# Optimization experiments

Measured on AMD Instinct MI355X. Metric: run time of the kernel, lower is better.

Reference implementation:

```python
import jax, jax.numpy as jnp
import numpy as np

N = 262144        # tokens routed
D = 1024          # input_dim
E = 64            # num_experts
TOP_K = 2
NOISE_EPS = 1e-05
ALPHA = 10.0


def setup_inputs() -> dict:
    key = jax.random.key(0)
    k1, k2, k3, k4, k5 = jax.random.split(key, 5)
    x = jax.random.normal(k1, (N, D), dtype=jnp.float32)
    # nn.Linear init scale ~ 1/sqrt(fan_in); keep logits at sane magnitude
    gate_w = jax.random.normal(k2, (E, D), dtype=jnp.float32) * (1.0 / np.sqrt(D))
    gate_b = jax.random.normal(k3, (E,), dtype=jnp.float32) * 0.01
    # w_noise is initialized to zeros in the module; use small random values
    # so the noise path is exercised
    w_noise = jax.random.normal(k4, (E, E), dtype=jnp.float32) * 0.01
    noise = jax.random.normal(k5, (N, E), dtype=jnp.float32)  # torch.randn_like
    return {"x": x, "gate_w": gate_w, "gate_b": gate_b,
            "w_noise": w_noise, "noise": noise}


def reference(x, gate_w, gate_b, w_noise, noise):
    # gate linear: [N, D] @ [D, E] + [E]
    clean_logits = jnp.einsum('nd,ed->ne', x, gate_w) + gate_b
    # training-mode learnable noise injection
    raw_noise_stddev = clean_logits @ w_noise                 # [N, E]
    noise_stddev = jax.nn.softplus(raw_noise_stddev) + NOISE_EPS
    logits = clean_logits + noise * noise_stddev              # noisy_logits

    # decompostion_tp: k-th largest per row (kthvalue(n - k + 1) == k-th largest)
    kth_largest = jax.lax.top_k(logits, TOP_K)[0][:, -1]       # [N]
    mask = logits < kth_largest[:, None]                       # strictly below kth
    sm = jax.nn.softmax(logits, axis=1)
    out = jnp.where(mask,
                    ALPHA * jnp.log1p(sm),      # alpha * log(sm + 1)
                    ALPHA * jnp.expm1(sm))      # alpha * (exp(sm) - 1)

    gates = jax.nn.softmax(out, axis=1)
    return gates
```

## Files before the change

kernel.cpp:

```cpp
#include <hip/hip_runtime.h>

typedef _Float16 half8v __attribute__((ext_vector_type(8)));
typedef float f32x4 __attribute__((ext_vector_type(4)));

constexpr float INV4096 = 1.0f / 4096.0f;
constexpr float ALPHA = 10.0f;

__device__ __forceinline__ f32x4 mfma16(half8v a, half8v b, f32x4 c_) {
  return __builtin_amdgcn_mfma_f32_16x16x32_f16(a, b, c_, 0, 0, 0);
}
__device__ __forceinline__ void dma16(const void *g, void *l) {
  __builtin_amdgcn_global_load_lds(
      (const __attribute__((address_space(1))) void *)g,
      (__attribute__((address_space(3))) void *)l, 16, 0, 0);
}
template <int N> __device__ __forceinline__ void wait_vm() {
  asm volatile("s_waitcnt vmcnt(%0)" ::"n"(N) : "memory");
}
#define FENCE() asm volatile("" ::: "memory")
#define BAR()                            \
  do {                                   \
    __builtin_amdgcn_s_barrier();        \
    __builtin_amdgcn_sched_barrier(0);   \
  } while (0)

__global__ __launch_bounds__(256) void presplit(const float *__restrict__ GW,
                                                const float *__restrict__ WN,
                                                char *__restrict__ ws) {
  const int b = blockIdx.x;
  const int tid = threadIdx.x;
  if (b < 64) {
    int idx = b * 256 + tid;
    int e = idx >> 8;
    int c4 = idx & 255;
    f32x4 v = *reinterpret_cast<const f32x4 *>(GW + (size_t)idx * 4);
#pragma unroll
    for (int j = 0; j < 4; ++j) {
      int k = c4 * 4 + j;
      float vv = v[j];
      _Float16 hh = (_Float16)vv;
      _Float16 ll = (_Float16)((vv - (float)hh) * 4096.0f);
      int ck = k >> 6, kk = k & 63;
      int off = ck * 16384 + e * 128 + ((((kk >> 3) ^ (e & 7))) << 4) + ((kk & 7) << 1);
      *reinterpret_cast<_Float16 *>(ws + off) = hh;
      *reinterpret_cast<_Float16 *>(ws + off + 8192) = ll;
    }
  } else {
    int idx = (b - 64) * 256 + tid;
    int k = idx >> 4;
    int e0 = (idx & 15) << 2;
    f32x4 v = *reinterpret_cast<const f32x4 *>(WN + (size_t)k * 64 + e0);
#pragma unroll
    for (int j = 0; j < 4; ++j) {
      int e = e0 + j;
      float vv = v[j];
      _Float16 hh = (_Float16)vv;
      _Float16 ll = (_Float16)((vv - (float)hh) * 4096.0f);
      int off = 262144 + e * 128 + ((((k >> 3) ^ (e & 7))) << 4) + ((k & 7) << 1);
      *reinterpret_cast<_Float16 *>(ws + off) = hh;
      *reinterpret_cast<_Float16 *>(ws + off + 8192) = ll;
    }
  }
}

__global__ __launch_bounds__(512, 4) void topk_gating(
    const float *__restrict__ X, const char *__restrict__ WS,
    const float *__restrict__ GB, const float *__restrict__ NZ,
    float *__restrict__ OUT) {
  __shared__ __align__(16) char lds[49152];
  const int tid = threadIdx.x;
  const int lane = tid & 63;
  const int wv = tid >> 6;
  const int q = lane >> 4;
  const int c = lane & 15;
  const int waveRow = blockIdx.x * 128 + wv * 16;

  f32x4 accH[4] = {};
  f32x4 accX[4] = {};
  f32x4 a0[4], a1[4];

  const float *xBase = X + (size_t)(waveRow + c) * 1024 + q * 8;
  const char *wsL = WS + wv * 2048 + lane * 16;

#define LDA4(dst, p)                        \
  {                                         \
    dst[0] = *(const f32x4 *)((p) + 0);     \
    dst[1] = *(const f32x4 *)((p) + 4);     \
    dst[2] = *(const f32x4 *)((p) + 32);    \
    dst[3] = *(const f32x4 *)((p) + 36);    \
  }
#define BDMA(CK)                                                      \
  {                                                                   \
    char *bd_ = lds + ((CK) % 3) * 16384 + wv * 2048;                 \
    dma16(wsL + (CK) * 16384, bd_);                                   \
    dma16(wsL + (CK) * 16384 + 1024, bd_ + 1024);                     \
  }
#define CONV(A, ah, al)                                           \
  {                                                               \
    _Pragma("unroll") for (int ks_ = 0; ks_ < 2; ++ks_)           \
        _Pragma("unroll") for (int j_ = 0; j_ < 8; ++j_) {        \
      float xv_ = A[ks_ * 2 + (j_ >> 2)][j_ & 3];                 \
      _Float16 hh_ = (_Float16)xv_;                               \
      ah[ks_][j_] = hh_;                                          \
      al[ks_][j_] = (_Float16)((xv_ - (float)hh_) * 4096.0f);     \
    }                                                             \
  }
#define MFMAB(BUF, ah, al)                                                 \
  {                                                                        \
    _Pragma("unroll") for (int ks_ = 0; ks_ < 2; ++ks_)                    \
        _Pragma("unroll") for (int t_ = 0; t_ < 4; ++t_) {                 \
      int e_ = t_ * 16 + c;                                                \
      int off_ = (BUF) + e_ * 128 + ((((ks_ * 4 + q) ^ (e_ & 7))) << 4);   \
      half8v bh_ = *reinterpret_cast<half8v *>(lds + off_);                \
      half8v bl_ = *reinterpret_cast<half8v *>(lds + off_ + 8192);         \
      accH[t_] = mfma16(ah[ks_], bh_, accH[t_]);                           \
      accX[t_] = mfma16(ah[ks_], bl_, accX[t_]);                           \
      accX[t_] = mfma16(al[ks_], bh_, accX[t_]);                           \
    }                                                                      \
  }
#define STEP(N, AC, AN)                                          \
  {                                                              \
    half8v ah[2], al[2];                                         \
    if ((N) + 1 <= 15) LDA4(AN, xBase + ((N) + 1) * 64);         \
    FENCE();                                                     \
    if ((N) + 2 <= 15) BDMA((N) + 2);                            \
    FENCE();                                                     \
    CONV(AC, ah, al);                                            \
    MFMAB(((N) % 3) * 16384, ah, al);                            \
  }

  BDMA(0); FENCE();
  LDA4(a0, xBase); FENCE();
  BDMA(1); FENCE();
  wait_vm<6>(); BAR();

  STEP(0, a0, a1)  wait_vm<6>(); BAR();
  STEP(1, a1, a0)  wait_vm<6>(); BAR();
  STEP(2, a0, a1)  wait_vm<6>(); BAR();
  STEP(3, a1, a0)  wait_vm<6>(); BAR();
  STEP(4, a0, a1)  wait_vm<6>(); BAR();
  STEP(5, a1, a0)  wait_vm<6>(); BAR();
  STEP(6, a0, a1)  wait_vm<6>(); BAR();
  STEP(7, a1, a0)  wait_vm<6>(); BAR();
  STEP(8, a0, a1)  wait_vm<6>(); BAR();
  STEP(9, a1, a0)  wait_vm<6>(); BAR();
  STEP(10, a0, a1) wait_vm<6>(); BAR();
  STEP(11, a1, a0) wait_vm<6>(); BAR();
  STEP(12, a0, a1) wait_vm<6>(); BAR();
  STEP(13, a1, a0) wait_vm<6>(); BAR();
  STEP(14, a0, a1) wait_vm<4>(); BAR();
  STEP(15, a1, a0)
  BAR();

  float bs0 = GB[c], bs1 = GB[16 + c], bs2 = GB[32 + c], bs3 = GB[48 + c];
  dma16(wsL + 262144, lds + 32768 + wv * 2048);
  dma16(wsL + 262144 + 1024, lds + 32768 + wv * 2048 + 1024);
  FENCE();
  float nz[4][4];
#pragma unroll
  for (int t = 0; t < 4; ++t)
#pragma unroll
    for (int r = 0; r < 4; ++r)
      nz[t][r] = NZ[(size_t)(waveRow + 4 * q + r) * 64 + t * 16 + c];

  float cl[4][4];
  const float bsv[4] = {bs0, bs1, bs2, bs3};
#pragma unroll
  for (int t = 0; t < 4; ++t)
#pragma unroll
    for (int r = 0; r < 4; ++r)
      cl[t][r] = accH[t][r] + accX[t][r] * INV4096 + bsv[t];

  char *cb = lds + wv * 4096;
#pragma unroll
  for (int t = 0; t < 4; ++t)
#pragma unroll
    for (int r = 0; r < 4; ++r) {
      int row = 4 * q + r;
      int colf = t * 16 + c;
      int off = row * 256 + ((((colf >> 2) ^ row)) << 4) + ((colf & 3) << 2);
      *reinterpret_cast<float *>(cb + off) = cl[t][r];
    }
  wait_vm<16>();
  BAR();

  f32x4 rH[4] = {};
  f32x4 rX[4] = {};
#pragma unroll
  for (int ks = 0; ks < 2; ++ks) {
    int slot0 = ks * 8 + q * 2;
    f32x4 va = *reinterpret_cast<f32x4 *>(cb + c * 256 + (((slot0 ^ c)) << 4));
    f32x4 vb = *reinterpret_cast<f32x4 *>(cb + c * 256 + ((((slot0 + 1) ^ c)) << 4));
    half8v ah, al;
#pragma unroll
    for (int j = 0; j < 4; ++j) {
      float v = va[j];
      _Float16 hh = (_Float16)v;
      ah[j] = hh;
      al[j] = (_Float16)((v - (float)hh) * 4096.0f);
      float v2 = vb[j];
      _Float16 h2 = (_Float16)v2;
      ah[4 + j] = h2;
      al[4 + j] = (_Float16)((v2 - (float)h2) * 4096.0f);
    }
#pragma unroll
    for (int t = 0; t < 4; ++t) {
      int e = t * 16 + c;
      int off = 32768 + e * 128 + ((((ks * 4 + q) ^ (e & 7))) << 4);
      half8v bh = *reinterpret_cast<half8v *>(lds + off);
      half8v bl = *reinterpret_cast<half8v *>(lds + off + 8192);
      rH[t] = mfma16(ah, bh, rH[t]);
      rX[t] = mfma16(ah, bl, rX[t]);
      rX[t] = mfma16(al, bh, rX[t]);
    }
  }

  float lg[4][4];
#pragma unroll
  for (int t = 0; t < 4; ++t)
#pragma unroll
    for (int r = 0; r < 4; ++r) {
      float raw = rH[t][r] + rX[t][r] * INV4096;
      float sp = fmaxf(raw, 0.0f) + __logf(1.0f + __expf(-fabsf(raw)));
      lg[r][t] = cl[t][r] + nz[t][r] * (sp + 1e-5f);
    }

#pragma unroll
  for (int r = 0; r < 4; ++r) {
    float v0 = lg[r][0], v1 = lg[r][1], v2 = lg[r][2], v3 = lg[r][3];
    float a = fmaxf(v0, v1), b_ = fminf(v0, v1);
    float d1 = fmaxf(v2, v3), d2 = fminf(v2, v3);
    float m1 = fmaxf(a, d1);
    float m2 = fmaxf(fminf(a, d1), fmaxf(b_, d2));
#pragma unroll
    for (int s = 1; s <= 8; s <<= 1) {
      float om1 = __shfl_xor(m1, s, 64);
      float om2 = __shfl_xor(m2, s, 64);
      float hi = fmaxf(m1, om1);
      float lo = fminf(m1, om1);
      float sec = (m1 >= om1) ? m2 : om2;
      m2 = fmaxf(lo, sec);
      m1 = hi;
    }
    float se[4], ssum = 0.f;
#pragma unroll
    for (int t = 0; t < 4; ++t) {
      se[t] = __expf(lg[r][t] - m1);
      ssum += se[t];
    }
#pragma unroll
    for (int s = 1; s <= 8; s <<= 1) ssum += __shfl_xor(ssum, s, 64);
    float inv = 1.0f / ssum;
    float ov[4];
#pragma unroll
    for (int t = 0; t < 4; ++t) {
      float sm = se[t] * inv;
      float vlog = ALPHA * __logf(1.0f + sm);
      float vexp = ALPHA * (__expf(sm) - 1.0f);
      ov[t] = (lg[r][t] < m2) ? vlog : vexp;
    }
    float g = fmaxf(fmaxf(ov[0], ov[1]), fmaxf(ov[2], ov[3]));
#pragma unroll
    for (int s = 1; s <= 8; s <<= 1) g = fmaxf(g, __shfl_xor(g, s, 64));
    float gsum = 0.f;
#pragma unroll
    for (int t = 0; t < 4; ++t) {
      ov[t] = __expf(ov[t] - g);
      gsum += ov[t];
    }
#pragma unroll
    for (int s = 1; s <= 8; s <<= 1) gsum += __shfl_xor(gsum, s, 64);
    float ginv = 1.0f / gsum;
    size_t rowOff = (size_t)(waveRow + 4 * q + r) * 64;
#pragma unroll
    for (int t = 0; t < 4; ++t)
      OUT[rowOff + t * 16 + c] = ov[t] * ginv;
  }
}

extern "C" void kernel_launch(void *const *d_in, const int *in_sizes, int n_in,
                              void *d_out, int out_size, void *d_ws,
                              size_t ws_size, hipStream_t stream) {
  const float *x = (const float *)d_in[0];
  const float *gw = (const float *)d_in[1];
  const float *gb = (const float *)d_in[2];
  const float *wn = (const float *)d_in[3];
  const float *nz = (const float *)d_in[4];
  float *out = (float *)d_out;
  char *ws = (char *)d_ws;
  const int N = in_sizes[0] / 1024;

  hipLaunchKernelGGL(presplit, dim3(68), dim3(256), 0, stream, gw, wn, ws);
  hipLaunchKernelGGL(topk_gating, dim3(N / 128), dim3(512), 0, stream, x, ws,
                     gb, nz, out);
}
```

Measured before the change: 270.5 us.

## Double-buffer 128-wide K chunks with half as many barriers

The K-loop now processes 128-element chunks in 8 steps instead of 64-element chunks in 16 steps. The weight tile is double-buffered in a 64KB LDS area instead of triple-buffered in 48KB, and the X tile is prefetched one step ahead into two register banks. Each block copies its whole weight chunk with thread-linear DMA addressing. This halves the barrier and waitcnt points per tile, which should cut synchronisation stalls. In exchange it raises per-block LDS and register use, which can lower the number of resident blocks per CU, and it shortens the weight prefetch distance from two steps to one.

```diff
diff --git a/kernel.cpp b/kernel.cpp
--- a/kernel.cpp
+++ b/kernel.cpp
@@ -67,7 +67,7 @@
     const float *__restrict__ X, const char *__restrict__ WS,
     const float *__restrict__ GB, const float *__restrict__ NZ,
     float *__restrict__ OUT) {
-  __shared__ __align__(16) char lds[49152];
+  __shared__ __align__(16) char lds[65536];
   const int tid = threadIdx.x;
   const int lane = tid & 63;
   const int wv = tid >> 6;
@@ -77,10 +77,10 @@
 
   f32x4 accH[4] = {};
   f32x4 accX[4] = {};
-  f32x4 a0[4], a1[4];
+  f32x4 aA[2][4], aB[2][4];
 
   const float *xBase = X + (size_t)(waveRow + c) * 1024 + q * 8;
-  const char *wsL = WS + wv * 2048 + lane * 16;
+  const char *wsT = WS + tid * 16;
 
 #define LDA4(dst, p)                        \
   {                                         \
@@ -89,11 +89,18 @@
     dst[2] = *(const f32x4 *)((p) + 32);    \
     dst[3] = *(const f32x4 *)((p) + 36);    \
   }
-#define BDMA(CK)                                                      \
-  {                                                                   \
-    char *bd_ = lds + ((CK) % 3) * 16384 + wv * 2048;                 \
-    dma16(wsL + (CK) * 16384, bd_);                                   \
-    dma16(wsL + (CK) * 16384 + 1024, bd_ + 1024);                     \
+#define LDAP(BANK, N)                       \
+  {                                         \
+    const float *p_ = xBase + (N) * 128;    \
+    LDA4(BANK[0], p_);                      \
+    LDA4(BANK[1], p_ + 64);                 \
+  }
+#define BDMA(N)                                                         \
+  {                                                                     \
+    char *bd_ = lds + ((N) % 2) * 32768;                                \
+    _Pragma("unroll") for (int i_ = 0; i_ < 4; ++i_)                    \
+        dma16(wsT + (N) * 32768 + i_ * 8192, bd_ + i_ * 8192 + tid * 16 \
+              - lane * 16);                                             \
   }
 #define CONV(A, ah, al)                                           \
   {                                                               \
@@ -118,43 +125,42 @@
       accX[t_] = mfma16(al[ks_], bh_, accX[t_]);                           \
     }                                                                      \
   }
-#define STEP(N, AC, AN)                                          \
-  {                                                              \
-    half8v ah[2], al[2];                                         \
-    if ((N) + 1 <= 15) LDA4(AN, xBase + ((N) + 1) * 64);         \
-    FENCE();                                                     \
-    if ((N) + 2 <= 15) BDMA((N) + 2);                            \
-    FENCE();                                                     \
-    CONV(AC, ah, al);                                            \
-    MFMAB(((N) % 3) * 16384, ah, al);                            \
+#define STEPC2(N, BANK)                                   \
+  {                                                       \
+    half8v ah[2], al[2];                                  \
+    CONV(BANK[0], ah, al);                                \
+    MFMAB(((N) % 2) * 32768, ah, al);                     \
+    CONV(BANK[1], ah, al);                                \
+    MFMAB(((N) % 2) * 32768 + 16384, ah, al);             \
+  }
+#define STEP(N, CUR, NXT)                                 \
+  {                                                       \
+    if ((N) + 1 <= 7) {                                   \
+      BDMA((N) + 1);                                      \
+      FENCE();                                            \
+      LDAP(NXT, (N) + 1);                                 \
+      FENCE();                                            \
+    }                                                     \
+    STEPC2(N, CUR);                                       \
   }
 
   BDMA(0); FENCE();
-  LDA4(a0, xBase); FENCE();
-  BDMA(1); FENCE();
-  wait_vm<6>(); BAR();
-
-  STEP(0, a0, a1)  wait_vm<6>(); BAR();
-  STEP(1, a1, a0)  wait_vm<6>(); BAR();
-  STEP(2, a0, a1)  wait_vm<6>(); BAR();
-  STEP(3, a1, a0)  wait_vm<6>(); BAR();
-  STEP(4, a0, a1)  wait_vm<6>(); BAR();
-  STEP(5, a1, a0)  wait_vm<6>(); BAR();
-  STEP(6, a0, a1)  wait_vm<6>(); BAR();
-  STEP(7, a1, a0)  wait_vm<6>(); BAR();
-  STEP(8, a0, a1)  wait_vm<6>(); BAR();
-  STEP(9, a1, a0)  wait_vm<6>(); BAR();
-  STEP(10, a0, a1) wait_vm<6>(); BAR();
-  STEP(11, a1, a0) wait_vm<6>(); BAR();
-  STEP(12, a0, a1) wait_vm<6>(); BAR();
-  STEP(13, a1, a0) wait_vm<6>(); BAR();
-  STEP(14, a0, a1) wait_vm<4>(); BAR();
-  STEP(15, a1, a0)
+  LDAP(aA, 0); FENCE();
+  wait_vm<8>(); BAR();
+
+  STEP(0, aA, aB) wait_vm<8>(); BAR();
+  STEP(1, aB, aA) wait_vm<8>(); BAR();
+  STEP(2, aA, aB) wait_vm<8>(); BAR();
+  STEP(3, aB, aA) wait_vm<8>(); BAR();
+  STEP(4, aA, aB) wait_vm<8>(); BAR();
+  STEP(5, aB, aA) wait_vm<8>(); BAR();
+  STEP(6, aA, aB) wait_vm<8>(); BAR();
+  STEP(7, aB, aA)
   BAR();
 
   float bs0 = GB[c], bs1 = GB[16 + c], bs2 = GB[32 + c], bs3 = GB[48 + c];
-  dma16(wsL + 262144, lds + 32768 + wv * 2048);
-  dma16(wsL + 262144 + 1024, lds + 32768 + wv * 2048 + 1024);
+  dma16(wsT + 262144, lds + 32768 + tid * 16 - lane * 16);
+  dma16(wsT + 262144 + 8192, lds + 32768 + 8192 + tid * 16 - lane * 16);
   FENCE();
   float nz[4][4];
 #pragma unroll
```

After: 259.1 us. 1.04x faster.
